# Performance work log

Measured on AMD Instinct MI355X. Metric: run time of the kernel, lower is better.

The kernel has to match this reference:

```python
import math
import jax, jax.numpy as jnp
import numpy as np

N_HEAD = 16

def setup_inputs() -> dict:
    key = jax.random.key(0)
    ks = jax.random.split(key, 7)
    B, T, C = 4, 2048, 1024
    QL, KVL = 256, 256
    s = 0.02
    return {
        "x":     jax.random.normal(ks[0], (B, T, C), jnp.float32),
        "W_dq":  jax.random.normal(ks[1], (QL, C), jnp.float32) * s,
        "W_uq":  jax.random.normal(ks[2], (C, QL), jnp.float32) * s,
        "W_dkv": jax.random.normal(ks[3], (KVL, C), jnp.float32) * s,
        "W_uk":  jax.random.normal(ks[4], (C, KVL), jnp.float32) * s,
        "W_uv":  jax.random.normal(ks[5], (C, KVL), jnp.float32) * s,
        "W_o":   jax.random.normal(ks[6], (C, C), jnp.float32) * s,
    }

def reference(x, W_dq, W_uq, W_dkv, W_uk, W_uv, W_o):
    B, T, C = x.shape
    nh = N_HEAD
    hs = C // nh
    kvl = W_dkv.shape[0]
    # Absorbed projection matrices (training path: recomputed each call)
    # k_eff: (nh, hs, kvl); v_eff: (nh, kvl, hs)
    k_eff = (W_dq.T @ W_uq.T @ W_uk).reshape(nh, hs, kvl)
    v_eff = (W_uv.T @ W_o.T).reshape(kvl, nh, hs).transpose(1, 0, 2)
    # Latent KV cache: (B, T, kvl)
    c_kv = x @ W_dkv.T
    # Queries: (B, nh, T, hs)
    q = (x @ W_dq.T @ W_uq.T).reshape(B, T, nh, hs).transpose(0, 2, 1, 3)
    # Scores: q @ k_eff @ c_kv^T / sqrt(hs) -> (B, nh, T, T)
    q_lat = jnp.einsum('bhtd,hdl->bhtl', q, k_eff)
    attn = jnp.einsum('bhtl,bsl->bhts', q_lat, c_kv) / math.sqrt(hs)
    causal_mask = jnp.triu(jnp.ones((T, T), bool), k=1)
    attn = jnp.where(causal_mask[None, None], -jnp.inf, attn)
    attn = jax.nn.softmax(attn, axis=-1)  # dropout p=0 -> identity
    # Output: attn @ c_kv @ v_eff -> (B, T, C)
    ctx = jnp.einsum('bhts,bsl->bhtl', attn, c_kv)
    y = jnp.einsum('bhtl,hld->bhtd', ctx, v_eff).transpose(0, 2, 1, 3).reshape(B, T, C)
    return (y, c_kv)
```

## Files before the change

kernel.cpp:

```cpp
#include <hip/hip_runtime.h>

typedef unsigned short u16;
typedef __attribute__((ext_vector_type(8))) short short8;
typedef __attribute__((ext_vector_type(4))) float f32x4;

#define MFMA_BF16 __builtin_amdgcn_mfma_f32_16x16x32_bf16

__device__ __forceinline__ u16 f2bf(float f){
  unsigned int u = __builtin_bit_cast(unsigned int, f);
  u += 0x7fffu + ((u >> 16) & 1u);
  return (u16)(u >> 16);
}

__device__ __forceinline__ void gld16(const void* g, void* l){
  __builtin_amdgcn_global_load_lds(
      (const __attribute__((address_space(1))) unsigned int*)g,
      (__attribute__((address_space(3))) unsigned int*)l, 16, 0, 0);
}

__global__ void k_transpose4(const float* __restrict__ s0, float* __restrict__ d0,
                             const float* __restrict__ s1, float* __restrict__ d1,
                             const float* __restrict__ s2, float* __restrict__ d2,
                             const float* __restrict__ s3, float* __restrict__ d3)
{
  __shared__ float tile[32][33];
  int z = blockIdx.z;
  const float* src = z == 0 ? s0 : z == 1 ? s1 : z == 2 ? s2 : s3;
  float* dst       = z == 0 ? d0 : z == 1 ? d1 : z == 2 ? d2 : d3;
  int rows = z == 0 ? 256 : 1024, cols = z == 0 ? 1024 : 256;
  int c0 = blockIdx.x * 32, r0 = blockIdx.y * 32;
  if (c0 >= cols || r0 >= rows) return;
  int tx = threadIdx.x, ty = threadIdx.y;
#pragma unroll
  for (int i = 0; i < 4; ++i){
    int r = ty + i * 8;
    tile[r][tx] = src[(long)(r0 + r) * cols + c0 + tx];
  }
  __syncthreads();
#pragma unroll
  for (int i = 0; i < 4; ++i){
    int r = ty + i * 8;
    dst[(long)(c0 + r) * rows + r0 + tx] = tile[tx][r];
  }
}

__global__ __launch_bounds__(256)
void k_gemm_nt(const float* __restrict__ A, const float* __restrict__ B,
               float* __restrict__ Cf, u16* __restrict__ Cb,
               int M, int N, int K, int lda, int ldb, int ldc,
               long sA, long sB, long sC, float scale)
{
  A += (long)blockIdx.z * sA; B += (long)blockIdx.z * sB;
  if (Cf) Cf += (long)blockIdx.z * sC;
  if (Cb) Cb += (long)blockIdx.z * sC;
  const int n0 = blockIdx.x * 64, m0 = blockIdx.y * 64;
  const int tid = threadIdx.x;
  const int wave = tid >> 6, lane = tid & 63, quad = lane >> 4, l16 = lane & 15;
  __shared__ u16 As[64 * 40];
  __shared__ u16 Bs[64 * 40];
  f32x4 acc[4];
#pragma unroll
  for (int n = 0; n < 4; ++n) acc[n] = (f32x4){0.f, 0.f, 0.f, 0.f};

  const int lr = tid >> 2;
  const int lc = (tid & 3) * 8;
  for (int k0 = 0; k0 < K; k0 += 32){
    {
      const float* pa = &A[(long)(m0 + lr) * lda + k0 + lc];
      float4 a0 = *(const float4*)pa;
      float4 a1 = *(const float4*)(pa + 4);
      short8 pk;
      pk[0]=(short)f2bf(a0.x); pk[1]=(short)f2bf(a0.y); pk[2]=(short)f2bf(a0.z); pk[3]=(short)f2bf(a0.w);
      pk[4]=(short)f2bf(a1.x); pk[5]=(short)f2bf(a1.y); pk[6]=(short)f2bf(a1.z); pk[7]=(short)f2bf(a1.w);
      *(short8*)&As[lr * 40 + lc] = pk;
      const float* pb = &B[(long)(n0 + lr) * ldb + k0 + lc];
      float4 b0 = *(const float4*)pb;
      float4 b1 = *(const float4*)(pb + 4);
      short8 qk;
      qk[0]=(short)f2bf(b0.x); qk[1]=(short)f2bf(b0.y); qk[2]=(short)f2bf(b0.z); qk[3]=(short)f2bf(b0.w);
      qk[4]=(short)f2bf(b1.x); qk[5]=(short)f2bf(b1.y); qk[6]=(short)f2bf(b1.z); qk[7]=(short)f2bf(b1.w);
      *(short8*)&Bs[lr * 40 + lc] = qk;
    }
    __syncthreads();
    short8 a = *(const short8*)&As[(wave * 16 + l16) * 40 + quad * 8];
#pragma unroll
    for (int n = 0; n < 4; ++n){
      short8 b = *(const short8*)&Bs[(n * 16 + l16) * 40 + quad * 8];
      acc[n] = MFMA_BF16(a, b, acc[n], 0, 0, 0);
    }
    __syncthreads();
  }
#pragma unroll
  for (int n = 0; n < 4; ++n)
#pragma unroll
    for (int r = 0; r < 4; ++r){
      int row = m0 + wave * 16 + quad * 4 + r;
      int col = n0 + n * 16 + l16;
      float v = acc[n][r] * scale;
      if (Cf) Cf[(long)row * ldc + col] = v;
      if (Cb) Cb[(long)row * ldc + col] = f2bf(v);
    }
}

__global__ __launch_bounds__(256)
void k_proj(const float* __restrict__ x, const float* __restrict__ Wdq,
            const float* __restrict__ Wdkv, u16* __restrict__ xq,
            float* __restrict__ ckv_f, u16* __restrict__ ckv_bf, u16* __restrict__ ckvT)
{
  const bool is_kv = blockIdx.x >= 4;
  const float* B = is_kv ? Wdkv : Wdq;
  const int n0 = (blockIdx.x & 3) * 64, m0 = blockIdx.y * 64;
  const int tid = threadIdx.x;
  const int wave = tid >> 6, lane = tid & 63, quad = lane >> 4, l16 = lane & 15;
  __shared__ u16 As[64 * 40];
  __shared__ u16 Bs[64 * 40];
  f32x4 acc[4];
#pragma unroll
  for (int n = 0; n < 4; ++n) acc[n] = (f32x4){0.f, 0.f, 0.f, 0.f};

  const int lr = tid >> 2;
  const int lc = (tid & 3) * 8;
  for (int k0 = 0; k0 < 1024; k0 += 32){
    {
      const float* pa = &x[(long)(m0 + lr) * 1024 + k0 + lc];
      float4 a0 = *(const float4*)pa;
      float4 a1 = *(const float4*)(pa + 4);
      short8 pk;
      pk[0]=(short)f2bf(a0.x); pk[1]=(short)f2bf(a0.y); pk[2]=(short)f2bf(a0.z); pk[3]=(short)f2bf(a0.w);
      pk[4]=(short)f2bf(a1.x); pk[5]=(short)f2bf(a1.y); pk[6]=(short)f2bf(a1.z); pk[7]=(short)f2bf(a1.w);
      *(short8*)&As[lr * 40 + lc] = pk;
      const float* pb = &B[(long)(n0 + lr) * 1024 + k0 + lc];
      float4 b0 = *(const float4*)pb;
      float4 b1 = *(const float4*)(pb + 4);
      short8 qk;
      qk[0]=(short)f2bf(b0.x); qk[1]=(short)f2bf(b0.y); qk[2]=(short)f2bf(b0.z); qk[3]=(short)f2bf(b0.w);
      qk[4]=(short)f2bf(b1.x); qk[5]=(short)f2bf(b1.y); qk[6]=(short)f2bf(b1.z); qk[7]=(short)f2bf(b1.w);
      *(short8*)&Bs[lr * 40 + lc] = qk;
    }
    __syncthreads();
    short8 a = *(const short8*)&As[(wave * 16 + l16) * 40 + quad * 8];
#pragma unroll
    for (int n = 0; n < 4; ++n){
      short8 b = *(const short8*)&Bs[(n * 16 + l16) * 40 + quad * 8];
      acc[n] = MFMA_BF16(a, b, acc[n], 0, 0, 0);
    }
    __syncthreads();
  }
  if (!is_kv){
#pragma unroll
    for (int n = 0; n < 4; ++n)
#pragma unroll
      for (int r = 0; r < 4; ++r){
        int row = m0 + wave * 16 + quad * 4 + r;
        int col = n0 + n * 16 + l16;
        xq[(long)row * 256 + col] = f2bf(acc[n][r]);
      }
  } else {
    const int b = (m0 >> 11);
    const int t0 = (m0 & 2047) + wave * 16 + quad * 4;
#pragma unroll
    for (int n = 0; n < 4; ++n){
      int col = n0 + n * 16 + l16;
      u16 pk[4];
#pragma unroll
      for (int r = 0; r < 4; ++r){
        int row = m0 + wave * 16 + quad * 4 + r;
        float v = acc[n][r];
        ckv_f [(long)row * 256 + col] = v;
        ckv_bf[(long)row * 256 + col] = f2bf(v);
        pk[r] = f2bf(v);
      }
      *(uint2*)&ckvT[((long)b * 256 + col) * 2048 + t0] = *(uint2*)pk;
    }
  }
}

__global__ __launch_bounds__(512, 2)
void k_flash(const u16* __restrict__ xq, const u16* __restrict__ Pt,
             const u16* __restrict__ ckv_bf, const u16* __restrict__ ckvT,
             const u16* __restrict__ Vt, float* __restrict__ y)
{
  const int bx = blockIdx.x;
  const int qt = (bx < 8) ? (15 - bx) : (bx - 8);
  const int h = blockIdx.y, b = blockIdx.z;
  const int tid = threadIdx.x;
  const int wg = tid >> 6, lane = tid & 63, quad = lane >> 4, l16 = lane & 15;

  __shared__ u16 LDS[73728];
  u16* PW = LDS + 65536 + wg * 1024;

  const int trow = wg * 16 + l16;
  const int swr  = l16 & 7;
  const long tglob = (long)b * 2048 + qt * 128;

  const u16* ckv_b  = ckv_bf + (long)b * 2048 * 256;
  const u16* ckvT_b = ckvT   + (long)b * 256 * 2048;

  int offA[4], offB[4];
  {
    int l5 = lane >> 5, g32 = lane & 31;
#pragma unroll
    for (int j = 0; j < 4; ++j){
      int s = (wg * 4 + j) * 2 + l5;
      offA[j] = s * 256 + ((g32 ^ (s & 7)) * 8);
    }
    int l3 = lane >> 3, g8 = lane & 7;
#pragma unroll
    for (int j = 0; j < 4; ++j){
      int l = (wg * 4 + j) * 8 + l3;
      offB[j] = l * 2048 + ((g8 ^ (l & 7)) * 8);
    }
  }

  short8 aS[8];
  {
    short8 bq[8];
    const u16* xr = xq + (tglob + trow) * 256;
#pragma unroll
    for (int ks = 0; ks < 8; ++ks)
      bq[ks] = *(const short8*)&xr[ks * 32 + quad * 8];
    const u16* pth = Pt + (long)h * 65536;
#pragma unroll
    for (int mb = 0; mb < 16; ++mb){
      f32x4 acc = (f32x4){0.f, 0.f, 0.f, 0.f};
#pragma unroll
      for (int ks = 0; ks < 8; ++ks){
        short8 pa = *(const short8*)&pth[(mb * 16 + l16) * 256 + ks * 32 + quad * 8];
        acc = MFMA_BF16(pa, bq[ks], acc, 0, 0, 0);
      }
#pragma unroll
      for (int r = 0; r < 4; ++r){
        int l = mb * 16 + quad * 4 + r;
        int cs = (((l >> 3) ^ swr) << 3) | (l & 7);
        LDS[trow * 256 + cs] = f2bf(acc[r]);
      }
    }
  }
  __syncthreads();
#pragma unroll
  for (int ks = 0; ks < 8; ++ks){
    int gl = ks * 4 + quad;
    aS[ks] = *(const short8*)&LDS[trow * 256 + ((gl ^ swr) << 3)];
  }
  __syncthreads();

#pragma unroll
  for (int j = 0; j < 4; ++j)
    gld16(ckv_b + offA[j], &LDS[(wg * 4 + j) * 512]);
#pragma unroll
  for (int j = 0; j < 4; ++j)
    gld16(ckvT_b + offB[j], &LDS[32768 + (wg * 4 + j) * 512]);

  float m_t = -1e30f, l_t = 0.f;
  f32x4 oacc[16];
#pragma unroll
  for (int n = 0; n < 16; ++n) oacc[n] = (f32x4){0.f, 0.f, 0.f, 0.f};

  const int stmax = 2 * qt + 1;
  const int tg = qt * 128 + trow;
  for (int st = 0; st <= stmax; ++st){
    const int cur = st & 1;
    __syncthreads();
    if (st < stmax){
      const int nx = cur ^ 1;
#pragma unroll
      for (int j = 0; j < 4; ++j)
        gld16(ckv_b + (long)(st + 1) * 16384 + offA[j],
              &LDS[nx * 16384 + (wg * 4 + j) * 512]);
#pragma unroll
      for (int j = 0; j < 4; ++j)
        gld16(ckvT_b + (st + 1) * 64 + offB[j],
              &LDS[32768 + nx * 16384 + (wg * 4 + j) * 512]);
    }
    if (st * 64 > qt * 128 + wg * 16 + 15) continue;

    const u16* X0 = LDS + cur * 16384;
    const u16* X1 = LDS + 32768 + cur * 16384;

    f32x4 sacc[4];
#pragma unroll
    for (int mb = 0; mb < 4; ++mb) sacc[mb] = (f32x4){0.f, 0.f, 0.f, 0.f};
    __builtin_amdgcn_s_setprio(1);
#pragma unroll
    for (int ks = 0; ks < 8; ++ks){
      int gl = ks * 4 + quad;
#pragma unroll
      for (int mb = 0; mb < 4; ++mb){
        short8 a = *(const short8*)&X0[(mb * 16 + l16) * 256 + ((gl ^ swr) << 3)];
        sacc[mb] = MFMA_BF16(a, aS[ks], sacc[mb], 0, 0, 0);
      }
    }
    __builtin_amdgcn_s_setprio(0);

    if (st * 64 + 63 > tg){
#pragma unroll
      for (int mb = 0; mb < 4; ++mb)
#pragma unroll
        for (int r = 0; r < 4; ++r)
          if (st * 64 + mb * 16 + quad * 4 + r > tg) sacc[mb][r] = -1e30f;
    }

    float rm = sacc[0][0];
#pragma unroll
    for (int mb = 0; mb < 4; ++mb)
#pragma unroll
      for (int r = 0; r < 4; ++r) rm = fmaxf(rm, sacc[mb][r]);
    rm = fmaxf(rm, __shfl_xor(rm, 16, 64));
    rm = fmaxf(rm, __shfl_xor(rm, 32, 64));
    if (!__all(rm <= m_t + 8.f)){
      float mnew = fmaxf(m_t, rm);
      float alpha = __expf(m_t - mnew);
      m_t = mnew;
      l_t *= alpha;
#pragma unroll
      for (int r2 = 0; r2 < 4; ++r2){
        float ar = __shfl(alpha, quad * 4 + r2, 64);
#pragma unroll
        for (int n = 0; n < 16; ++n) oacc[n][r2] *= ar;
      }
    }
    float rs = 0.f;
#pragma unroll
    for (int mb = 0; mb < 4; ++mb){
      float p0 = __expf(sacc[mb][0] - m_t);
      float p1 = __expf(sacc[mb][1] - m_t);
      float p2 = __expf(sacc[mb][2] - m_t);
      float p3 = __expf(sacc[mb][3] - m_t);
      rs += (p0 + p1) + (p2 + p3);
      unsigned int w0 = (unsigned)f2bf(p0) | ((unsigned)f2bf(p1) << 16);
      unsigned int w1 = (unsigned)f2bf(p2) | ((unsigned)f2bf(p3) << 16);
      int pos = (2 * mb + (quad >> 1)) ^ swr;
      uint2 w; w.x = w0; w.y = w1;
      *(uint2*)&PW[l16 * 64 + pos * 8 + (quad & 1) * 4] = w;
    }
    rs += __shfl_xor(rs, 16, 64);
    rs += __shfl_xor(rs, 32, 64);
    l_t += rs;

    short8 a0 = *(const short8*)&PW[l16 * 64 + ((quad ^ swr) << 3)];
    short8 a1 = *(const short8*)&PW[l16 * 64 + (((4 + quad) ^ swr) << 3)];
    __builtin_amdgcn_s_setprio(1);
#pragma unroll
    for (int n = 0; n < 16; ++n){
      int lr_ = n * 16 + l16;
      int swl = lr_ & 7;
      short8 b0 = *(const short8*)&X1[lr_ * 64 + ((quad ^ swl) << 3)];
      short8 b1 = *(const short8*)&X1[lr_ * 64 + (((4 + quad) ^ swl) << 3)];
      oacc[n] = MFMA_BF16(a0, b0, oacc[n], 0, 0, 0);
      oacc[n] = MFMA_BF16(a1, b1, oacc[n], 0, 0, 0);
    }
    __builtin_amdgcn_s_setprio(0);
  }

  __syncthreads();
  {
    float linv = 1.f / l_t;
#pragma unroll
    for (int r = 0; r < 4; ++r){
      float lr_ = __shfl(linv, quad * 4 + r, 64);
#pragma unroll
      for (int n = 0; n < 16; ++n) oacc[n][r] *= lr_;
    }
#pragma unroll
    for (int n = 0; n < 16; ++n)
#pragma unroll
      for (int r = 0; r < 4; ++r){
        int trw = wg * 16 + quad * 4 + r;
        int l = n * 16 + l16;
        int cs = (((l >> 3) ^ (trw & 7)) << 3) | (l & 7);
        LDS[trw * 256 + cs] = f2bf(oacc[n][r]);
      }
  }
  __syncthreads();
  {
    const u16* vth = Vt + (long)h * 64 * 256;
    short8 ca[8];
#pragma unroll
    for (int ks = 0; ks < 8; ++ks){
      int gl = ks * 4 + quad;
      ca[ks] = *(const short8*)&LDS[trow * 256 + ((gl ^ swr) << 3)];
    }
#pragma unroll
    for (int n = 0; n < 4; ++n){
      f32x4 acc = (f32x4){0.f, 0.f, 0.f, 0.f};
#pragma unroll
      for (int ks = 0; ks < 8; ++ks){
        short8 vb = *(const short8*)&vth[(n * 16 + l16) * 256 + ks * 32 + quad * 8];
        acc = MFMA_BF16(ca[ks], vb, acc, 0, 0, 0);
      }
#pragma unroll
      for (int r = 0; r < 4; ++r)
        y[(tglob + wg * 16 + quad * 4 + r) * 1024 + h * 64 + n * 16 + l16] = acc[r];
    }
  }
}

extern "C" void kernel_launch(void* const* d_in, const int* in_sizes, int n_in,
                              void* d_out, int out_size, void* d_ws, size_t ws_size,
                              hipStream_t stream)
{
  (void)in_sizes; (void)n_in; (void)out_size; (void)ws_size;
  const float* x    = (const float*)d_in[0];
  const float* Wdq  = (const float*)d_in[1];
  const float* Wuq  = (const float*)d_in[2];
  const float* Wdkv = (const float*)d_in[3];
  const float* Wuk  = (const float*)d_in[4];
  const float* Wuv  = (const float*)d_in[5];
  const float* Wo   = (const float*)d_in[6];

  float* y_out   = (float*)d_out;
  float* ckv_out = y_out + (size_t)4 * 2048 * 1024;

  char* base = (char*)d_ws;
  float* wdqT   = (float*)(base + 0);
  float* wuqT   = (float*)(base + 1048576);
  float* wukT   = (float*)(base + 2097152);
  float* wuvT   = (float*)(base + 3145728);
  u16*   ckvT   = (u16*)  (base + 0);
  float* t1T    = (float*)(base + 4194304);
  float* keffT  = (float*)(base + 4456448);
  u16*   pt     = (u16*)  (base + 5505024);
  u16*   vt     = (u16*)  (base + 7602176);
  u16*   xq     = (u16*)  (base + 8126464);
  u16*   ckv_bf = (u16*)  (base + 12320768);

  k_transpose4<<<dim3(32, 32, 4), dim3(32, 8), 0, stream>>>(
      Wdq, wdqT, Wuq, wuqT, Wuk, wukT, Wuv, wuvT);

  k_gemm_nt<<<dim3(4, 4, 1), 256, 0, stream>>>(wukT, wuqT, t1T, (u16*)0,
      256, 256, 1024, 1024, 1024, 256, 0, 0, 0, 1.f);
  k_gemm_nt<<<dim3(16, 4, 1), 256, 0, stream>>>(t1T, wdqT, keffT, (u16*)0,
      256, 1024, 256, 256, 256, 1024, 0, 0, 0, 1.f);
  k_gemm_nt<<<dim3(4, 4, 16), 256, 0, stream>>>(keffT, wuqT, (float*)0, pt,
      256, 256, 64, 1024, 1024, 256, 64, 64, 65536, 0.125f);
  k_gemm_nt<<<dim3(4, 16, 1), 256, 0, stream>>>(Wo, wuvT, (float*)0, vt,
      1024, 256, 1024, 1024, 1024, 256, 0, 0, 0, 1.f);

  k_proj<<<dim3(8, 128), 256, 0, stream>>>(x, Wdq, Wdkv, xq, ckv_out, ckv_bf, ckvT);

  k_flash<<<dim3(16, 16, 4), 512, 0, stream>>>(xq, pt, ckv_bf, ckvT, vt, y_out);
}
```

Before: 690.3 us.

## Switch flash attention inner loop to 32x32x16 MFMA with register-resident P

Recasts the attention loop to use 32x32x16 bf16 MFMA tiles. Each pair of waves owns 32 query rows and recomputes the same score tile, then splits the 256-wide latent output between them. The probability matrix is packed to bf16 and exchanged through cross-lane shuffles instead of a per-wave LDS staging buffer, which removes that buffer and shrinks LDS use. The cost is duplicated QK^T MFMA work per wave pair, coarser causal skipping, and different register pressure for the larger accumulators.

After: 745.3 us. 8.0% more time.

```diff
diff --git a/kernel.cpp b/kernel.cpp
--- a/kernel.cpp
+++ b/kernel.cpp
@@ -3,13 +3,20 @@
 typedef unsigned short u16;
 typedef __attribute__((ext_vector_type(8))) short short8;
 typedef __attribute__((ext_vector_type(4))) float f32x4;
+typedef __attribute__((ext_vector_type(16))) float f32x16;
+typedef __attribute__((ext_vector_type(4))) unsigned int u32x4;
 
 #define MFMA_BF16 __builtin_amdgcn_mfma_f32_16x16x32_bf16
+#define MFMA32    __builtin_amdgcn_mfma_f32_32x32x16_bf16
 
 __device__ __forceinline__ u16 f2bf(float f){
   unsigned int u = __builtin_bit_cast(unsigned int, f);
   u += 0x7fffu + ((u >> 16) & 1u);
   return (u16)(u >> 16);
+}
+
+__device__ __forceinline__ unsigned int pk2(float a, float b){
+  return (unsigned)f2bf(a) | ((unsigned)f2bf(b) << 16);
 }
 
 __device__ __forceinline__ void gld16(const void* g, void* l){
@@ -185,9 +192,10 @@
   const int h = blockIdx.y, b = blockIdx.z;
   const int tid = threadIdx.x;
   const int wg = tid >> 6, lane = tid & 63, quad = lane >> 4, l16 = lane & 15;
-
-  __shared__ u16 LDS[73728];
-  u16* PW = LDS + 65536 + wg * 1024;
+  const int lid = lane & 31, hi = lane >> 5;
+  const int ts = wg >> 1, lh = wg & 1;
+
+  __shared__ u16 LDS[65536];
 
   const int trow = wg * 16 + l16;
   const int swr  = l16 & 7;
@@ -212,21 +220,20 @@
     }
   }
 
-  short8 aS[8];
   {
-    short8 bq[8];
+    short8 bq0[8];
     const u16* xr = xq + (tglob + trow) * 256;
 #pragma unroll
     for (int ks = 0; ks < 8; ++ks)
-      bq[ks] = *(const short8*)&xr[ks * 32 + quad * 8];
+      bq0[ks] = *(const short8*)&xr[ks * 32 + quad * 8];
     const u16* pth = Pt + (long)h * 65536;
 #pragma unroll
     for (int mb = 0; mb < 16; ++mb){
       f32x4 acc = (f32x4){0.f, 0.f, 0.f, 0.f};
 #pragma unroll
       for (int ks = 0; ks < 8; ++ks){
-        short8 pa = *(const short8*)&pth[(mb * 16 + l16) * 256 + ks * 32 + quad * 8];
-        acc = MFMA_BF16(pa, bq[ks], acc, 0, 0, 0);
+        short8 pa_ = *(const short8*)&pth[(mb * 16 + l16) * 256 + ks * 32 + quad * 8];
+        acc = MFMA_BF16(pa_, bq0[ks], acc, 0, 0, 0);
       }
 #pragma unroll
       for (int r = 0; r < 4; ++r){
@@ -237,10 +244,13 @@
     }
   }
   __syncthreads();
-#pragma unroll
-  for (int ks = 0; ks < 8; ++ks){
-    int gl = ks * 4 + quad;
-    aS[ks] = *(const short8*)&LDS[trow * 256 + ((gl ^ swr) << 3)];
+  short8 bq[16];
+  {
+    const int tr = ts * 32 + lid;
+    const int swt = tr & 7;
+#pragma unroll
+    for (int ks = 0; ks < 16; ++ks)
+      bq[ks] = *(const short8*)&LDS[tr * 256 + (((2 * ks + hi) ^ swt) << 3)];
   }
   __syncthreads();
 
@@ -252,12 +262,14 @@
     gld16(ckvT_b + offB[j], &LDS[32768 + (wg * 4 + j) * 512]);
 
   float m_t = -1e30f, l_t = 0.f;
-  f32x4 oacc[16];
-#pragma unroll
-  for (int n = 0; n < 16; ++n) oacc[n] = (f32x4){0.f, 0.f, 0.f, 0.f};
+  f32x16 oacc[4];
+#pragma unroll
+  for (int n = 0; n < 4; ++n)
+#pragma unroll
+    for (int r = 0; r < 16; ++r) oacc[n][r] = 0.f;
 
   const int stmax = 2 * qt + 1;
-  const int tg = qt * 128 + trow;
+  const int tq = qt * 128 + ts * 32 + lid;
   for (int st = 0; st <= stmax; ++st){
     const int cur = st & 1;
     __syncthreads();
@@ -272,40 +284,40 @@
         gld16(ckvT_b + (st + 1) * 64 + offB[j],
               &LDS[32768 + nx * 16384 + (wg * 4 + j) * 512]);
     }
-    if (st * 64 > qt * 128 + wg * 16 + 15) continue;
-
-    const u16* X0 = LDS + cur * 16384;
-    const u16* X1 = LDS + 32768 + cur * 16384;
-
-    f32x4 sacc[4];
-#pragma unroll
-    for (int mb = 0; mb < 4; ++mb) sacc[mb] = (f32x4){0.f, 0.f, 0.f, 0.f};
+    if (st * 64 > qt * 128 + ts * 32 + 31) continue;
+
+    const u16* X0c = LDS + cur * 16384;
+    const u16* X1c = LDS + 32768 + cur * 16384;
+
+    f32x16 sacc0, sacc1;
+#pragma unroll
+    for (int r = 0; r < 16; ++r){ sacc0[r] = 0.f; sacc1[r] = 0.f; }
+    const int swl0 = lid & 7;
     __builtin_amdgcn_s_setprio(1);
 #pragma unroll
-    for (int ks = 0; ks < 8; ++ks){
-      int gl = ks * 4 + quad;
-#pragma unroll
-      for (int mb = 0; mb < 4; ++mb){
-        short8 a = *(const short8*)&X0[(mb * 16 + l16) * 256 + ((gl ^ swr) << 3)];
-        sacc[mb] = MFMA_BF16(a, aS[ks], sacc[mb], 0, 0, 0);
-      }
+    for (int ks = 0; ks < 16; ++ks){
+      int g = 2 * ks + hi;
+      short8 a0 = *(const short8*)&X0c[lid * 256 + ((g ^ swl0) << 3)];
+      short8 a1 = *(const short8*)&X0c[(32 + lid) * 256 + ((g ^ swl0) << 3)];
+      sacc0 = MFMA32(a0, bq[ks], sacc0, 0, 0, 0);
+      sacc1 = MFMA32(a1, bq[ks], sacc1, 0, 0, 0);
     }
     __builtin_amdgcn_s_setprio(0);
 
-    if (st * 64 + 63 > tg){
-#pragma unroll
-      for (int mb = 0; mb < 4; ++mb)
-#pragma unroll
-        for (int r = 0; r < 4; ++r)
-          if (st * 64 + mb * 16 + quad * 4 + r > tg) sacc[mb][r] = -1e30f;
-    }
-
-    float rm = sacc[0][0];
-#pragma unroll
-    for (int mb = 0; mb < 4; ++mb)
-#pragma unroll
-      for (int r = 0; r < 4; ++r) rm = fmaxf(rm, sacc[mb][r]);
-    rm = fmaxf(rm, __shfl_xor(rm, 16, 64));
+    if (st * 64 + 63 > qt * 128 + ts * 32){
+#pragma unroll
+      for (int r = 0; r < 16; ++r){
+        int sb = (r & 3) + 8 * (r >> 2) + 4 * hi;
+        if (st * 64 + sb > tq)      sacc0[r] = -1e30f;
+        if (st * 64 + 32 + sb > tq) sacc1[r] = -1e30f;
+      }
+    }
+
+    float rm = sacc0[0];
+#pragma unroll
+    for (int r = 1; r < 16; ++r) rm = fmaxf(rm, sacc0[r]);
+#pragma unroll
+    for (int r = 0; r < 16; ++r) rm = fmaxf(rm, sacc1[r]);
     rm = fmaxf(rm, __shfl_xor(rm, 32, 64));
     if (!__all(rm <= m_t + 8.f)){
       float mnew = fmaxf(m_t, rm);
@@ -313,41 +325,52 @@
       m_t = mnew;
       l_t *= alpha;
 #pragma unroll
-      for (int r2 = 0; r2 < 4; ++r2){
-        float ar = __shfl(alpha, quad * 4 + r2, 64);
-#pragma unroll
-        for (int n = 0; n < 16; ++n) oacc[n][r2] *= ar;
+      for (int r = 0; r < 16; ++r){
+        float ar = __shfl(alpha, (r & 3) + 8 * (r >> 2) + 4 * hi, 64);
+#pragma unroll
+        for (int n = 0; n < 4; ++n) oacc[n][r] *= ar;
       }
     }
     float rs = 0.f;
 #pragma unroll
-    for (int mb = 0; mb < 4; ++mb){
-      float p0 = __expf(sacc[mb][0] - m_t);
-      float p1 = __expf(sacc[mb][1] - m_t);
-      float p2 = __expf(sacc[mb][2] - m_t);
-      float p3 = __expf(sacc[mb][3] - m_t);
-      rs += (p0 + p1) + (p2 + p3);
-      unsigned int w0 = (unsigned)f2bf(p0) | ((unsigned)f2bf(p1) << 16);
-      unsigned int w1 = (unsigned)f2bf(p2) | ((unsigned)f2bf(p3) << 16);
-      int pos = (2 * mb + (quad >> 1)) ^ swr;
-      uint2 w; w.x = w0; w.y = w1;
-      *(uint2*)&PW[l16 * 64 + pos * 8 + (quad & 1) * 4] = w;
-    }
-    rs += __shfl_xor(rs, 16, 64);
+    for (int r = 0; r < 16; ++r){
+      float e0 = __expf(sacc0[r] - m_t); sacc0[r] = e0; rs += e0;
+      float e1 = __expf(sacc1[r] - m_t); sacc1[r] = e1; rs += e1;
+    }
     rs += __shfl_xor(rs, 32, 64);
     l_t += rs;
 
-    short8 a0 = *(const short8*)&PW[l16 * 64 + ((quad ^ swr) << 3)];
-    short8 a1 = *(const short8*)&PW[l16 * 64 + (((4 + quad) ^ swr) << 3)];
+    short8 pa[4];
+#pragma unroll
+    for (int kk = 0; kk < 4; ++kk){
+      f32x16 Pv = (kk < 2) ? sacc0 : sacc1;
+      int rb = (kk & 1) * 8;
+      unsigned wa0 = pk2(Pv[rb + 0], Pv[rb + 1]);
+      unsigned wa1 = pk2(Pv[rb + 2], Pv[rb + 3]);
+      unsigned wb0 = pk2(Pv[rb + 4], Pv[rb + 5]);
+      unsigned wb1 = pk2(Pv[rb + 6], Pv[rb + 7]);
+      unsigned W1 = hi ? wa0 : wb0;
+      unsigned W2 = hi ? wa1 : wb1;
+      unsigned R1 = (unsigned)__shfl_xor((int)W1, 32, 64);
+      unsigned R2 = (unsigned)__shfl_xor((int)W2, 32, 64);
+      u32x4 v;
+      v.x = hi ? R1 : wa0;
+      v.y = hi ? R2 : wa1;
+      v.z = hi ? wb0 : R1;
+      v.w = hi ? wb1 : R2;
+      pa[kk] = __builtin_bit_cast(short8, v);
+    }
+
     __builtin_amdgcn_s_setprio(1);
 #pragma unroll
-    for (int n = 0; n < 16; ++n){
-      int lr_ = n * 16 + l16;
-      int swl = lr_ & 7;
-      short8 b0 = *(const short8*)&X1[lr_ * 64 + ((quad ^ swl) << 3)];
-      short8 b1 = *(const short8*)&X1[lr_ * 64 + (((4 + quad) ^ swl) << 3)];
-      oacc[n] = MFMA_BF16(a0, b0, oacc[n], 0, 0, 0);
-      oacc[n] = MFMA_BF16(a1, b1, oacc[n], 0, 0, 0);
+    for (int nt = 0; nt < 4; ++nt){
+      int lrow = lh * 128 + nt * 32 + lid;
+      int sw = lrow & 7;
+#pragma unroll
+      for (int kk = 0; kk < 4; ++kk){
+        short8 bfr = *(const short8*)&X1c[lrow * 64 + (((2 * kk + hi) ^ sw) << 3)];
+        oacc[nt] = MFMA32(pa[kk], bfr, oacc[nt], 0, 0, 0);
+      }
     }
     __builtin_amdgcn_s_setprio(0);
   }
@@ -356,19 +379,19 @@
   {
     float linv = 1.f / l_t;
 #pragma unroll
-    for (int r = 0; r < 4; ++r){
-      float lr_ = __shfl(linv, quad * 4 + r, 64);
-#pragma unroll
-      for (int n = 0; n < 16; ++n) oacc[n][r] *= lr_;
-    }
-#pragma unroll
-    for (int n = 0; n < 16; ++n)
-#pragma unroll
-      for (int r = 0; r < 4; ++r){
-        int trw = wg * 16 + quad * 4 + r;
-        int l = n * 16 + l16;
-        int cs = (((l >> 3) ^ (trw & 7)) << 3) | (l & 7);
-        LDS[trw * 256 + cs] = f2bf(oacc[n][r]);
+    for (int r = 0; r < 16; ++r){
+      float lr_ = __shfl(linv, (r & 3) + 8 * (r >> 2) + 4 * hi, 64);
+#pragma unroll
+      for (int n = 0; n < 4; ++n) oacc[n][r] *= lr_;
+    }
+#pragma unroll
+    for (int nt = 0; nt < 4; ++nt)
+#pragma unroll
+      for (int r = 0; r < 16; ++r){
+        int tl = ts * 32 + (r & 3) + 8 * (r >> 2) + 4 * hi;
+        int l = lh * 128 + nt * 32 + lid;
+        int cs = (((l >> 3) ^ (tl & 7)) << 3) | (l & 7);
+        LDS[tl * 256 + cs] = f2bf(oacc[nt][r]);
       }
   }
   __syncthreads();
```

## Restructure projection GEMM so each block covers all 512 output columns

Applied to the files above, without the earlier changes.

The x projection kernel now uses 256 blocks of 512 threads. Each block owns 32 rows and computes both the query and KV latent outputs (all 512 columns) at once, so x is read and converted to bf16 once per row instead of being re-read by 8 column blocks. The cost moves to the weights: every block now streams the full Wdq and Wdkv (512x1024) and converts them to bf16, with a larger LDS footprint and fewer blocks.

Result: slower. 728.2 us (+5.5%).

```diff
diff --git a/kernel.cpp b/kernel.cpp
--- a/kernel.cpp
+++ b/kernel.cpp
@@ -102,75 +102,76 @@
     }
 }
 
-__global__ __launch_bounds__(256)
-void k_proj(const float* __restrict__ x, const float* __restrict__ Wdq,
-            const float* __restrict__ Wdkv, u16* __restrict__ xq,
-            float* __restrict__ ckv_f, u16* __restrict__ ckv_bf, u16* __restrict__ ckvT)
+__global__ __launch_bounds__(512)
+void k_proj2(const float* __restrict__ x, const float* __restrict__ Wdq,
+             const float* __restrict__ Wdkv, u16* __restrict__ xq,
+             float* __restrict__ ckv_f, u16* __restrict__ ckv_bf, u16* __restrict__ ckvT)
 {
-  const bool is_kv = blockIdx.x >= 4;
-  const float* B = is_kv ? Wdkv : Wdq;
-  const int n0 = (blockIdx.x & 3) * 64, m0 = blockIdx.y * 64;
+  const int m0 = blockIdx.x * 32;
   const int tid = threadIdx.x;
-  const int wave = tid >> 6, lane = tid & 63, quad = lane >> 4, l16 = lane & 15;
-  __shared__ u16 As[64 * 40];
-  __shared__ u16 Bs[64 * 40];
-  f32x4 acc[4];
-#pragma unroll
-  for (int n = 0; n < 4; ++n) acc[n] = (f32x4){0.f, 0.f, 0.f, 0.f};
-
-  const int lr = tid >> 2;
-  const int lc = (tid & 3) * 8;
+  const int w = tid >> 6, lane = tid & 63, quad = lane >> 4, l16 = lane & 15;
+  const int rs = (w & 1) * 16, cq = w >> 1;
+
+  __shared__ u16 As[32 * 40];
+  __shared__ u16 Bs[512 * 40];
+
+  f32x4 acc[8];
+#pragma unroll
+  for (int n = 0; n < 8; ++n) acc[n] = (f32x4){0.f, 0.f, 0.f, 0.f};
+
+  const float* brow = (tid < 256) ? (Wdq + (long)tid * 1024)
+                                  : (Wdkv + (long)(tid - 256) * 1024);
+  const int ar = tid >> 4;
+  const int ac = (tid & 15) * 2;
+
   for (int k0 = 0; k0 < 1024; k0 += 32){
     {
-      const float* pa = &x[(long)(m0 + lr) * 1024 + k0 + lc];
-      float4 a0 = *(const float4*)pa;
-      float4 a1 = *(const float4*)(pa + 4);
-      short8 pk;
-      pk[0]=(short)f2bf(a0.x); pk[1]=(short)f2bf(a0.y); pk[2]=(short)f2bf(a0.z); pk[3]=(short)f2bf(a0.w);
-      pk[4]=(short)f2bf(a1.x); pk[5]=(short)f2bf(a1.y); pk[6]=(short)f2bf(a1.z); pk[7]=(short)f2bf(a1.w);
-      *(short8*)&As[lr * 40 + lc] = pk;
-      const float* pb = &B[(long)(n0 + lr) * 1024 + k0 + lc];
-      float4 b0 = *(const float4*)pb;
-      float4 b1 = *(const float4*)(pb + 4);
-      short8 qk;
-      qk[0]=(short)f2bf(b0.x); qk[1]=(short)f2bf(b0.y); qk[2]=(short)f2bf(b0.z); qk[3]=(short)f2bf(b0.w);
-      qk[4]=(short)f2bf(b1.x); qk[5]=(short)f2bf(b1.y); qk[6]=(short)f2bf(b1.z); qk[7]=(short)f2bf(b1.w);
-      *(short8*)&Bs[lr * 40 + lc] = qk;
+      float2 a2 = *(const float2*)&x[(long)(m0 + ar) * 1024 + k0 + ac];
+      As[ar * 40 + ac]     = f2bf(a2.x);
+      As[ar * 40 + ac + 1] = f2bf(a2.y);
+#pragma unroll
+      for (int q = 0; q < 4; ++q){
+        float4 bv = *(const float4*)&brow[k0 + q * 8];
+        float4 bw = *(const float4*)&brow[k0 + q * 8 + 4];
+        short8 pk;
+        pk[0]=(short)f2bf(bv.x); pk[1]=(short)f2bf(bv.y); pk[2]=(short)f2bf(bv.z); pk[3]=(short)f2bf(bv.w);
+        pk[4]=(short)f2bf(bw.x); pk[5]=(short)f2bf(bw.y); pk[6]=(short)f2bf(bw.z); pk[7]=(short)f2bf(bw.w);
+        *(short8*)&Bs[tid * 40 + q * 8] = pk;
+      }
     }
     __syncthreads();
-    short8 a = *(const short8*)&As[(wave * 16 + l16) * 40 + quad * 8];
-#pragma unroll
-    for (int n = 0; n < 4; ++n){
-      short8 b = *(const short8*)&Bs[(n * 16 + l16) * 40 + quad * 8];
+    short8 a = *(const short8*)&As[(rs + l16) * 40 + quad * 8];
+#pragma unroll
+    for (int n = 0; n < 8; ++n){
+      short8 b = *(const short8*)&Bs[(cq * 128 + n * 16 + l16) * 40 + quad * 8];
       acc[n] = MFMA_BF16(a, b, acc[n], 0, 0, 0);
     }
     __syncthreads();
   }
-  if (!is_kv){
-#pragma unroll
-    for (int n = 0; n < 4; ++n)
+
+  const int bb = m0 >> 11;
+  const int t0 = (m0 & 2047) + rs + quad * 4;
+#pragma unroll
+  for (int n = 0; n < 8; ++n){
+    int colW = cq * 128 + n * 16 + l16;
+    if (colW < 256){
 #pragma unroll
       for (int r = 0; r < 4; ++r){
-        int row = m0 + wave * 16 + quad * 4 + r;
-        int col = n0 + n * 16 + l16;
-        xq[(long)row * 256 + col] = f2bf(acc[n][r]);
-      }
-  } else {
-    const int b = (m0 >> 11);
-    const int t0 = (m0 & 2047) + wave * 16 + quad * 4;
-#pragma unroll
-    for (int n = 0; n < 4; ++n){
-      int col = n0 + n * 16 + l16;
+        int row = m0 + rs + quad * 4 + r;
+        xq[(long)row * 256 + colW] = f2bf(acc[n][r]);
+      }
+    } else {
+      int c = colW - 256;
       u16 pk[4];
 #pragma unroll
       for (int r = 0; r < 4; ++r){
-        int row = m0 + wave * 16 + quad * 4 + r;
+        int row = m0 + rs + quad * 4 + r;
         float v = acc[n][r];
-        ckv_f [(long)row * 256 + col] = v;
-        ckv_bf[(long)row * 256 + col] = f2bf(v);
+        ckv_f [(long)row * 256 + c] = v;
+        ckv_bf[(long)row * 256 + c] = f2bf(v);
         pk[r] = f2bf(v);
       }
-      *(uint2*)&ckvT[((long)b * 256 + col) * 2048 + t0] = *(uint2*)pk;
+      *(uint2*)&ckvT[((long)bb * 256 + c) * 2048 + t0] = *(uint2*)pk;
     }
   }
 }
@@ -436,7 +437,7 @@
   k_gemm_nt<<<dim3(4, 16, 1), 256, 0, stream>>>(Wo, wuvT, (float*)0, vt,
       1024, 256, 1024, 1024, 1024, 256, 0, 0, 0, 1.f);
 
-  k_proj<<<dim3(8, 128), 256, 0, stream>>>(x, Wdq, Wdkv, xq, ckv_out, ckv_bf, ckvT);
+  k_proj2<<<dim3(256), 512, 0, stream>>>(x, Wdq, Wdkv, xq, ckv_out, ckv_bf, ckvT);
 
   k_flash<<<dim3(16, 16, 4), 512, 0, stream>>>(xq, pt, ckv_bf, ckvT, vt, y_out);
 }
```
